# Kernel tuning notes

Hardware: AMD Instinct MI355X
Metric: run time of the kernel (lower is better)

Reference implementation:

```python
import jax, jax.numpy as jnp
import numpy as np

B, N, D = 1, 4096, 3072
H, DH = 16, 64
INNER = H * DH  # 1024
SCALE = DH ** -0.5
EPS = 1e-5


def setup_inputs() -> dict:
    key = jax.random.key(0)
    ks = jax.random.split(key, 4)
    x = jax.random.normal(ks[0], (B, N, D), jnp.float32)
    pe = jax.random.normal(ks[1], (1, 1, N, DH // 2, 2, 2), jnp.float32)
    w_qkv = jax.random.normal(ks[2], (3 * INNER, D), jnp.float32) * 0.02
    w_out = jax.random.normal(ks[3], (D, INNER), jnp.float32) * 0.02
    ln_g = jnp.ones((D,), jnp.float32)
    ln_b = jnp.zeros((D,), jnp.float32)
    return {"x": x, "pe": pe, "w_qkv": w_qkv, "w_out": w_out, "ln_g": ln_g, "ln_b": ln_b}


def _apply_rope(t, pe):
    # t: [b,h,n,d], pe: [1,1,n,d/2,2,2] (Flux rope layout)
    b, h, n, d = t.shape
    t_ = t.reshape(b, h, n, d // 2, 1, 2)
    out = pe[..., 0] * t_[..., 0] + pe[..., 1] * t_[..., 1]  # [b,h,n,d/2,2]
    return out.reshape(b, h, n, d)


def reference(x, pe, w_qkv, w_out, ln_g, ln_b):
    # LayerNorm (norm2)
    mu = jnp.mean(x, axis=-1, keepdims=True)
    var = jnp.mean((x - mu) ** 2, axis=-1, keepdims=True)
    xn = (x - mu) / jnp.sqrt(var + EPS) * ln_g + ln_b
    # QKV projection (no bias)
    qkv = xn @ w_qkv.T  # [b,n,3*inner]
    q, k, v = jnp.split(qkv, 3, axis=-1)
    def split_heads(t):
        return t.reshape(B, N, H, DH).transpose(0, 2, 1, 3)  # b h n d
    q, k, v = split_heads(q), split_heads(k), split_heads(v)
    # RoPE on q and k (attention_aug_bbox with mask=None, aug idx = -1 -> plain rope attn)
    q = _apply_rope(q, pe)
    k = _apply_rope(k, pe)
    scores = jnp.einsum('bhqd,bhkd->bhqk', q, k) * SCALE
    attn = jax.nn.softmax(scores, axis=-1)
    o = jnp.einsum('bhqk,bhkd->bhqd', attn, v)
    o = o.transpose(0, 2, 1, 3).reshape(B, N, INNER)  # b n (h d)
    return o @ w_out.T  # [b,n,dim]
```

## Files before the change

### kernel.cpp

```cpp
#include <hip/hip_runtime.h>
#include <hip/hip_bf16.h>

typedef unsigned short u16;
typedef __attribute__((ext_vector_type(8))) short bf16x8;
typedef __attribute__((ext_vector_type(4))) float f32x4;

#define N_TOK 4096
#define DMODEL 3072
#define NH 16
#define DHEAD 64
#define INNER 1024
#define SCALE_LOG2E 0.18033688011112042f

__device__ __forceinline__ u16 f2bf(float f) {
    union { float f; unsigned u; } un; un.f = f;
    unsigned r = un.u + 0x7fffu + ((un.u >> 16) & 1u);
    return (u16)(r >> 16);
}
__device__ __forceinline__ float bf2f(u16 u) {
    union { unsigned u; float f; } x; x.u = ((unsigned)u) << 16; return x.f;
}
__device__ __forceinline__ unsigned pk2bf(float a, float b) {
    union { float f; unsigned u; } ua, ub; ua.f = a; ub.f = b;
    return __builtin_amdgcn_perm(ub.u + 0x8000u, ua.u + 0x8000u, 0x07060302u);
}
__device__ __forceinline__ void load_lds16(const u16* g, u16* l) {
    __builtin_amdgcn_global_load_lds(
        (const __attribute__((address_space(1))) unsigned int*)g,
        (__attribute__((address_space(3))) unsigned int*)l, 16, 0, 0);
}

__global__ __launch_bounds__(256) void ln_kernel(const float* __restrict__ x,
                                                 const float* __restrict__ g,
                                                 const float* __restrict__ b,
                                                 u16* __restrict__ xn) {
    int row = blockIdx.x;
    int tid = threadIdx.x;
    const float4* xr = (const float4*)(x + (size_t)row * DMODEL);
    float4 v[3];
    float s = 0.f, ss = 0.f;
#pragma unroll
    for (int i = 0; i < 3; ++i) {
        v[i] = xr[i * 256 + tid];
        s  += v[i].x + v[i].y + v[i].z + v[i].w;
        ss += v[i].x * v[i].x + v[i].y * v[i].y + v[i].z * v[i].z + v[i].w * v[i].w;
    }
#pragma unroll
    for (int off = 32; off; off >>= 1) {
        s  += __shfl_xor(s, off);
        ss += __shfl_xor(ss, off);
    }
    __shared__ float red[8];
    int wid = tid >> 6, lane = tid & 63;
    if (lane == 0) { red[wid] = s; red[wid + 4] = ss; }
    __syncthreads();
    s  = red[0] + red[1] + red[2] + red[3];
    ss = red[4] + red[5] + red[6] + red[7];
    float mean = s * (1.f / DMODEL);
    float var  = ss * (1.f / DMODEL) - mean * mean;
    float rstd = rsqrtf(var + 1e-5f);
    ushort4* orow = (ushort4*)(xn + (size_t)row * DMODEL);
#pragma unroll
    for (int i = 0; i < 3; ++i) {
        float4 gg = ((const float4*)g)[i * 256 + tid];
        float4 bb = ((const float4*)b)[i * 256 + tid];
        ushort4 o;
        o.x = f2bf((v[i].x - mean) * rstd * gg.x + bb.x);
        o.y = f2bf((v[i].y - mean) * rstd * gg.y + bb.y);
        o.z = f2bf((v[i].z - mean) * rstd * gg.z + bb.z);
        o.w = f2bf((v[i].w - mean) * rstd * gg.w + bb.w);
        orow[i * 256 + tid] = o;
    }
}

__global__ __launch_bounds__(256) void cvt_bf16(const float* __restrict__ in,
                                                u16* __restrict__ out, int n4) {
    int i = blockIdx.x * 256 + threadIdx.x;
    if (i < n4) {
        float4 v = ((const float4*)in)[i];
        ushort4 o;
        o.x = f2bf(v.x); o.y = f2bf(v.y); o.z = f2bf(v.z); o.w = f2bf(v.w);
        ((ushort4*)out)[i] = o;
    }
}


#define VM6 asm volatile("s_waitcnt vmcnt(6)" ::: "memory")
#define VM0 asm volatile("s_waitcnt vmcnt(0)" ::: "memory")
#define LGK8 asm volatile("s_waitcnt lgkmcnt(8)" ::: "memory")
#define NOPS ((void)0)

#define ST_A(d, h, t) do { \
    load_lds16(pA##h##0 + (size_t)(t) * 64, &lds[(d) * 16384 + (h) * 8192 + dq]); \
    load_lds16(pA##h##1 + (size_t)(t) * 64, &lds[(d) * 16384 + (h) * 8192 + dq + 512]); \
  } while (0)
#define ST_B(d, h, t) do { \
    load_lds16(pB##h##0 + (size_t)(t) * 64, &lds[32768 + (d) * 16384 + (h) * 8192 + dq]); \
    load_lds16(pB##h##1 + (size_t)(t) * 64, &lds[32768 + (d) * 16384 + (h) * 8192 + dq + 512]); \
  } while (0)

#define PHASE(d, p, STAGE, PRE, POST) do { \
    bf16x8 afr[2][2]; \
    if ((p) == 0) { \
      _Pragma("unroll") for (int nf = 0; nf < 4; ++nf) { \
        bfr[nf][0] = *(const bf16x8*)&lds[(d) * 16384 + baseB + nf * 1024 + c0]; \
        bfr[nf][1] = *(const bf16x8*)&lds[(d) * 16384 + baseB + nf * 1024 + c1]; \
      } \
    } \
    _Pragma("unroll") for (int mfl = 0; mfl < 2; ++mfl) { \
      afr[mfl][0] = *(const bf16x8*)&lds[(d) * 16384 + (p) * 4096 + mfl * 1024 + baseA + c0]; \
      afr[mfl][1] = *(const bf16x8*)&lds[(d) * 16384 + (p) * 4096 + mfl * 1024 + baseA + c1]; \
    } \
    STAGE; \
    PRE; \
    __builtin_amdgcn_s_barrier(); \
    asm volatile("s_waitcnt lgkmcnt(0)" ::: "memory"); \
    __builtin_amdgcn_sched_barrier(0); \
    __builtin_amdgcn_s_setprio(1); \
    _Pragma("unroll") for (int mfl = 0; mfl < 2; ++mfl) \
      _Pragma("unroll") for (int nf = 0; nf < 4; ++nf) { \
        acc[(p) * 2 + mfl][nf] = __builtin_amdgcn_mfma_f32_16x16x32_bf16(afr[mfl][0], bfr[nf][0], acc[(p) * 2 + mfl][nf], 0, 0, 0); \
        acc[(p) * 2 + mfl][nf] = __builtin_amdgcn_mfma_f32_16x16x32_bf16(afr[mfl][1], bfr[nf][1], acc[(p) * 2 + mfl][nf], 0, 0, 0); \
      } \
    __builtin_amdgcn_s_setprio(0); \
    POST; \
    __builtin_amdgcn_s_barrier(); \
  } while (0)

template <int CBF16>
__global__ __launch_bounds__(512, 2) void gemm256(const u16* __restrict__ A,
                                                  const u16* __restrict__ B,
                                                  void* __restrict__ C,
                                                  int M, int Nn, int K) {
    __shared__ u16 lds[65536];
    const int tid = threadIdx.x;
    const int lane = tid & 63, wid = tid >> 6;
    const int wm = wid >> 2, wn = wid & 3;
    const int l15 = lane & 15, quad = lane >> 4;
    const int sw = l15 & 7;

    int nbx = Nn >> 8;
    int cpx = gridDim.x >> 3;
    int wg = (blockIdx.x & 7) * cpx + (blockIdx.x >> 3);
    int m0 = (wg / nbx) << 8, n0 = (wg % nbx) << 8;

    const int baseA = wm * 2048 + l15 * 64;
    const int baseB = 32768 + wn * 4096 + l15 * 64;
    const int c0 = (quad ^ sw) * 8;
    const int c1 = ((4 + quad) ^ sw) * 8;
    const int dq = wid * 1024;

    const u16 *pA00, *pA01, *pA10, *pA11, *pB00, *pB01, *pB10, *pB11;
    {
        int scol = ((lane & 7) ^ (lane >> 3)) * 8;
#define MKSRC(h, j, PA, PB) { \
        int ell = (h) * 128 + (wid * 2 + (j)) * 8 + (lane >> 3); \
        int g = ell >> 6, wmh = (ell >> 5) & 1, r = ell & 31; \
        PA = A + (size_t)(m0 + wmh * 128 + g * 32 + r) * K + scol; \
        PB = B + (size_t)(n0 + ell) * K + scol; }
        MKSRC(0, 0, pA00, pB00) MKSRC(0, 1, pA01, pB01)
        MKSRC(1, 0, pA10, pB10) MKSRC(1, 1, pA11, pB11)
#undef MKSRC
    }

    f32x4 acc[8][4];
    f32x4 zero4 = {0.f, 0.f, 0.f, 0.f};
#pragma unroll
    for (int i = 0; i < 8; ++i)
#pragma unroll
        for (int j = 0; j < 4; ++j) acc[i][j] = zero4;
    bf16x8 bfr[4][2];

    ST_B(0, 0, 0); ST_B(0, 1, 0); ST_A(0, 0, 0); ST_A(0, 1, 0);
    ST_B(1, 0, 1); ST_B(1, 1, 1); ST_A(1, 0, 1);
    VM6;
    __builtin_amdgcn_s_barrier();

    const int NIT = (K >> 7) - 1;
    for (int i = 0; i < NIT; ++i) {
        int t = 2 * i;
        PHASE(0, 0, ST_A(1, 1, t + 1), LGK8, NOPS);
        PHASE(0, 1, ST_B(0, 0, t + 2), NOPS, NOPS);
        PHASE(0, 2, ST_B(0, 1, t + 2), NOPS, NOPS);
        PHASE(0, 3, ST_A(0, 0, t + 2), NOPS, VM6);
        PHASE(1, 0, ST_A(0, 1, t + 2), LGK8, NOPS);
        PHASE(1, 1, ST_B(1, 0, t + 3), NOPS, NOPS);
        PHASE(1, 2, ST_B(1, 1, t + 3), NOPS, NOPS);
        PHASE(1, 3, ST_A(1, 0, t + 3), NOPS, VM6);
    }
    {
        int T = K >> 6;
        PHASE(0, 0, ST_A(1, 1, T - 1), LGK8, NOPS);
        PHASE(0, 1, NOPS, NOPS, NOPS);
        PHASE(0, 2, NOPS, NOPS, NOPS);
        PHASE(0, 3, NOPS, NOPS, VM0);
        PHASE(1, 0, NOPS, LGK8, NOPS);
        PHASE(1, 1, NOPS, NOPS, NOPS);
        PHASE(1, 2, NOPS, NOPS, NOPS);
        PHASE(1, 3, NOPS, NOPS, NOPS);
    }

#pragma unroll
    for (int mf = 0; mf < 8; ++mf)
#pragma unroll
        for (int nf = 0; nf < 4; ++nf)
#pragma unroll
            for (int r = 0; r < 4; ++r) {
                int rr = m0 + wm * 128 + mf * 16 + quad * 4 + r;
                int cc = n0 + wn * 64 + nf * 16 + l15;
                if (CBF16)
                    ((u16*)C)[(size_t)rr * Nn + cc] = f2bf(acc[mf][nf][r]);
                else
                    ((float*)C)[(size_t)rr * Nn + cc] = acc[mf][nf][r];
            }
}

__global__ __launch_bounds__(256) void rope_qk(const u16* __restrict__ qkv,
                                               const float* __restrict__ pe,
                                               u16* __restrict__ Qr,
                                               u16* __restrict__ Kr) {
    int n = blockIdx.x;
    int tid = threadIdx.x;
    const u16* qrow = qkv + (size_t)n * DMODEL;
    const float4* pen = (const float4*)(pe + (size_t)n * 128);
#pragma unroll
    for (int it = 0; it < 2; ++it) {
        int p = it * 256 + tid;
        int h = p >> 5, i = p & 31;
        float4 w = pen[i];
        size_t obase = ((size_t)h * N_TOK + n) * DHEAD + 2 * i;
        unsigned qq = *(const unsigned*)&qrow[h * 64 + 2 * i];
        float q0 = bf2f((u16)qq), q1 = bf2f((u16)(qq >> 16));
        *(unsigned*)&Qr[obase] = pk2bf((w.x * q0 + w.y * q1) * SCALE_LOG2E,
                                       (w.z * q0 + w.w * q1) * SCALE_LOG2E);
        unsigned kk = *(const unsigned*)&qrow[INNER + h * 64 + 2 * i];
        float k0 = bf2f((u16)kk), k1 = bf2f((u16)(kk >> 16));
        *(unsigned*)&Kr[obase] = pk2bf(w.x * k0 + w.y * k1, w.z * k0 + w.w * k1);
    }
}

__global__ __launch_bounds__(256) void v_transpose(const u16* __restrict__ qkv,
                                                   u16* __restrict__ Vt) {
    __shared__ u16 t[64][65];
    int n0 = blockIdx.x * 64;
    int h = blockIdx.y;
    int tid = threadIdx.x;
#pragma unroll
    for (int it = 0; it < 4; ++it) {
        int nr = it * 16 + (tid >> 4);
        int dc = (tid & 15) * 4;
        ushort4 v = *(const ushort4*)&qkv[(size_t)(n0 + nr) * DMODEL + 2 * INNER + h * 64 + dc];
        t[dc + 0][nr] = v.x; t[dc + 1][nr] = v.y; t[dc + 2][nr] = v.z; t[dc + 3][nr] = v.w;
    }
    __syncthreads();
#pragma unroll
    for (int it = 0; it < 4; ++it) {
        int dr = it * 16 + (tid >> 4);
        int nc = (tid & 15) * 4;
        ushort4 v;
        v.x = t[dr][nc]; v.y = t[dr][nc + 1]; v.z = t[dr][nc + 2]; v.w = t[dr][nc + 3];
        *(ushort4*)&Vt[((size_t)h * 64 + dr) * N_TOK + n0 + nc] = v;
    }
}

__global__ __launch_bounds__(256, 2) void flash_attn(const u16* __restrict__ Q,
                                                     const u16* __restrict__ K,
                                                     const u16* __restrict__ Vt,
                                                     u16* __restrict__ O) {
    __shared__ u16 lds_all[16384];
    u16* Ks = lds_all;
    u16* Vs = lds_all + 4096;
    int tid = threadIdx.x, lane = tid & 63, wid = tid >> 6;
    u16* Ps = lds_all + 8192 + wid * 2048;
    int l15 = lane & 15, quad = lane >> 4;
    int sw = l15 & 7;
    int h = blockIdx.y;
    int q0 = blockIdx.x * 128 + wid * 32;
    const u16* Qh = Q + (size_t)h * N_TOK * DHEAD;
    const u16* Kh = K + (size_t)h * N_TOK * DHEAD;
    const u16* Vh = Vt + (size_t)h * DHEAD * N_TOK;

    f32x4 zero4 = {0.f, 0.f, 0.f, 0.f};
    bf16x8 ones;
#pragma unroll
    for (int i = 0; i < 8; ++i) ones[i] = (short)0x3F80;

    bf16x8 aq[2][2];
#pragma unroll
    for (int mtQ = 0; mtQ < 2; ++mtQ)
#pragma unroll
        for (int kc = 0; kc < 2; ++kc)
            aq[mtQ][kc] = *(const bf16x8*)&Qh[(size_t)(q0 + mtQ * 16 + l15) * DHEAD + kc * 32 + quad * 8];

    f32x4 o[2][4], lacc[2];
#pragma unroll
    for (int mtQ = 0; mtQ < 2; ++mtQ) {
#pragma unroll
        for (int dt = 0; dt < 4; ++dt) o[mtQ][dt] = zero4;
        lacc[mtQ] = zero4;
    }

    int rbase = wid * 16;
    int rowoff = lane >> 3;
    int csw = ((lane & 7) ^ rowoff) * 8;

    for (int kt = 0; kt < N_TOK; kt += 64) {
        load_lds16(&Kh[(size_t)(kt + rbase + rowoff) * DHEAD + csw], &Ks[rbase * 64]);
        load_lds16(&Kh[(size_t)(kt + rbase + 8 + rowoff) * DHEAD + csw], &Ks[(rbase + 8) * 64]);
        load_lds16(&Vh[(size_t)(rbase + rowoff) * N_TOK + kt + csw], &Vs[rbase * 64]);
        load_lds16(&Vh[(size_t)(rbase + 8 + rowoff) * N_TOK + kt + csw], &Vs[(rbase + 8) * 64]);
        __syncthreads();

        bf16x8 bk[4][2], av[4][2];
#pragma unroll
        for (int t = 0; t < 4; ++t)
#pragma unroll
            for (int kc = 0; kc < 2; ++kc) {
                int off = (t * 16 + l15) * 64 + (((kc * 4 + quad) ^ sw) * 8);
                bk[t][kc] = *(const bf16x8*)&Ks[off];
                av[t][kc] = *(const bf16x8*)&Vs[off];
            }
        __syncthreads();

#pragma unroll
        for (int mtQ = 0; mtQ < 2; ++mtQ) {
            f32x4 s[4];
#pragma unroll
            for (int ntK = 0; ntK < 4; ++ntK) {
                f32x4 t0 = __builtin_amdgcn_mfma_f32_16x16x32_bf16(bk[ntK][0], aq[mtQ][0], zero4, 0, 0, 0);
                s[ntK] = __builtin_amdgcn_mfma_f32_16x16x32_bf16(bk[ntK][1], aq[mtQ][1], t0, 0, 0, 0);
            }
#pragma unroll
            for (int ntK = 0; ntK < 4; ++ntK) {
                uint2 pv;
                pv.x = pk2bf(__builtin_amdgcn_exp2f(s[ntK][0]), __builtin_amdgcn_exp2f(s[ntK][1]));
                pv.y = pk2bf(__builtin_amdgcn_exp2f(s[ntK][2]), __builtin_amdgcn_exp2f(s[ntK][3]));
                int pc = (ntK * 2 + (quad >> 1)) ^ sw;
                *(uint2*)&Ps[(mtQ * 16 + l15) * 64 + pc * 8 + (quad & 1) * 4] = pv;
            }
            bf16x8 bp0 = *(const bf16x8*)&Ps[(mtQ * 16 + l15) * 64 + ((quad ^ sw) * 8)];
            bf16x8 bp1 = *(const bf16x8*)&Ps[(mtQ * 16 + l15) * 64 + (((4 + quad) ^ sw) * 8)];
            lacc[mtQ] = __builtin_amdgcn_mfma_f32_16x16x32_bf16(ones, bp0, lacc[mtQ], 0, 0, 0);
            lacc[mtQ] = __builtin_amdgcn_mfma_f32_16x16x32_bf16(ones, bp1, lacc[mtQ], 0, 0, 0);
#pragma unroll
            for (int dt = 0; dt < 4; ++dt) {
                o[mtQ][dt] = __builtin_amdgcn_mfma_f32_16x16x32_bf16(av[dt][0], bp0, o[mtQ][dt], 0, 0, 0);
                o[mtQ][dt] = __builtin_amdgcn_mfma_f32_16x16x32_bf16(av[dt][1], bp1, o[mtQ][dt], 0, 0, 0);
            }
        }
    }

    __syncthreads();
    u16* scratch = lds_all + wid * 2048;
#pragma unroll
    for (int mtQ = 0; mtQ < 2; ++mtQ) {
        float rl = 1.f / lacc[mtQ][0];
#pragma unroll
        for (int dt = 0; dt < 4; ++dt) {
            uint2 ov;
            ov.x = pk2bf(o[mtQ][dt][0] * rl, o[mtQ][dt][1] * rl);
            ov.y = pk2bf(o[mtQ][dt][2] * rl, o[mtQ][dt][3] * rl);
            *(uint2*)&scratch[(mtQ * 16 + l15) * 64 + dt * 16 + quad * 4] = ov;
        }
    }
#pragma unroll
    for (int p = 0; p < 4; ++p) {
        int q_local = p * 8 + (lane >> 3);
        int dcol = (lane & 7) * 8;
        bf16x8 v = *(const bf16x8*)&scratch[q_local * 64 + dcol];
        *(bf16x8*)&O[(size_t)(q0 + q_local) * INNER + h * 64 + dcol] = v;
    }
}

extern "C" void kernel_launch(void* const* d_in, const int* in_sizes, int n_in,
                              void* d_out, int out_size, void* d_ws, size_t ws_size,
                              hipStream_t stream) {
    const float* x     = (const float*)d_in[0];
    const float* pe    = (const float*)d_in[1];
    const float* w_qkv = (const float*)d_in[2];
    const float* w_out = (const float*)d_in[3];
    const float* ln_g  = (const float*)d_in[4];
    const float* ln_b  = (const float*)d_in[5];
    float* out = (float*)d_out;

    char* ws = (char*)d_ws;
    u16* xn  = (u16*)ws;  ws += (size_t)N_TOK * DMODEL * 2;
    u16* wq  = (u16*)ws;  ws += (size_t)3 * INNER * DMODEL * 2;
    u16* wo  = (u16*)ws;  ws += (size_t)DMODEL * INNER * 2;
    u16* qkv = (u16*)ws;  ws += (size_t)N_TOK * DMODEL * 2;
    u16* Qr  = (u16*)ws;  ws += (size_t)NH * N_TOK * DHEAD * 2;
    u16* Kr  = (u16*)ws;  ws += (size_t)NH * N_TOK * DHEAD * 2;
    u16* Vt  = (u16*)ws;  ws += (size_t)NH * DHEAD * N_TOK * 2;
    u16* Ob  = (u16*)ws;  ws += (size_t)N_TOK * INNER * 2;

    ln_kernel<<<N_TOK, 256, 0, stream>>>(x, ln_g, ln_b, xn);
    {
        int n4 = 3 * INNER * DMODEL / 4;
        cvt_bf16<<<(n4 + 255) / 256, 256, 0, stream>>>(w_qkv, wq, n4);
    }
    {
        int n4 = DMODEL * INNER / 4;
        cvt_bf16<<<(n4 + 255) / 256, 256, 0, stream>>>(w_out, wo, n4);
    }
    gemm256<1><<<dim3((N_TOK / 256) * (DMODEL / 256)), 512, 0, stream>>>(xn, wq, qkv, N_TOK, DMODEL, DMODEL);
    rope_qk<<<N_TOK, 256, 0, stream>>>(qkv, pe, Qr, Kr);
    v_transpose<<<dim3(N_TOK / 64, NH), 256, 0, stream>>>(qkv, Vt);
    flash_attn<<<dim3(N_TOK / 128, NH), 256, 0, stream>>>(Qr, Kr, Vt, Ob);
    gemm256<0><<<dim3((N_TOK / 256) * (DMODEL / 256)), 512, 0, stream>>>(Ob, wo, out, N_TOK, DMODEL, INNER);
}
```

Before: 375.4 us.

## Double-buffer K/V tiles in flash attention with async prefetch

Flash attention now uses two LDS buffers for K/V tiles and prefetches the tile two steps ahead while the current tile is computed. Explicit vmcnt and lgkmcnt waits with raw s_barrier calls replace the two __syncthreads per iteration. The goal is to hide global-to-LDS load latency behind the MFMA and exp work. LDS usage grows from 32KB to 48KB per block, which could limit occupancy at two blocks per CU.

```diff
diff --git a/kernel.cpp b/kernel.cpp
--- a/kernel.cpp
+++ b/kernel.cpp
@@ -86,6 +86,7 @@
 
 
 #define VM6 asm volatile("s_waitcnt vmcnt(6)" ::: "memory")
+#define VM4 asm volatile("s_waitcnt vmcnt(4)" ::: "memory")
 #define VM0 asm volatile("s_waitcnt vmcnt(0)" ::: "memory")
 #define LGK8 asm volatile("s_waitcnt lgkmcnt(8)" ::: "memory")
 #define NOPS ((void)0)
@@ -263,15 +264,61 @@
     }
 }
 
+
+#define FA_STAGE(d, kt) do { \
+    load_lds16(&Kh[(size_t)((kt) + rbase + rowoff) * DHEAD + csw], &lds_all[(d) * 8192 + rbase * 64]); \
+    load_lds16(&Kh[(size_t)((kt) + rbase + 8 + rowoff) * DHEAD + csw], &lds_all[(d) * 8192 + (rbase + 8) * 64]); \
+    load_lds16(&Vh[(size_t)(rbase + rowoff) * N_TOK + (kt) + csw], &lds_all[(d) * 8192 + 4096 + rbase * 64]); \
+    load_lds16(&Vh[(size_t)(rbase + 8 + rowoff) * N_TOK + (kt) + csw], &lds_all[(d) * 8192 + 4096 + (rbase + 8) * 64]); \
+  } while (0)
+
+#define FA_TILE(d, STAGE_STMT, WAIT_STMT) do { \
+    bf16x8 bk[4][2], av[4][2]; \
+    _Pragma("unroll") for (int tt = 0; tt < 4; ++tt) \
+      _Pragma("unroll") for (int kc = 0; kc < 2; ++kc) { \
+        int off = (d) * 8192 + (tt * 16 + l15) * 64 + (((kc * 4 + quad) ^ sw) * 8); \
+        bk[tt][kc] = *(const bf16x8*)&lds_all[off]; \
+        av[tt][kc] = *(const bf16x8*)&lds_all[off + 4096]; \
+      } \
+    asm volatile("s_waitcnt lgkmcnt(0)" ::: "memory"); \
+    __builtin_amdgcn_sched_barrier(0); \
+    __builtin_amdgcn_s_barrier(); \
+    __builtin_amdgcn_sched_barrier(0); \
+    STAGE_STMT; \
+    _Pragma("unroll") for (int mtQ = 0; mtQ < 2; ++mtQ) { \
+      f32x4 s[4]; \
+      _Pragma("unroll") for (int ntK = 0; ntK < 4; ++ntK) { \
+        f32x4 t0 = __builtin_amdgcn_mfma_f32_16x16x32_bf16(bk[ntK][0], aq[mtQ][0], zero4, 0, 0, 0); \
+        s[ntK] = __builtin_amdgcn_mfma_f32_16x16x32_bf16(bk[ntK][1], aq[mtQ][1], t0, 0, 0, 0); \
+      } \
+      _Pragma("unroll") for (int ntK = 0; ntK < 4; ++ntK) { \
+        uint2 pv; \
+        pv.x = pk2bf(__builtin_amdgcn_exp2f(s[ntK][0]), __builtin_amdgcn_exp2f(s[ntK][1])); \
+        pv.y = pk2bf(__builtin_amdgcn_exp2f(s[ntK][2]), __builtin_amdgcn_exp2f(s[ntK][3])); \
+        int pc = (ntK * 2 + (quad >> 1)) ^ sw; \
+        *(uint2*)&Ps[(mtQ * 16 + l15) * 64 + pc * 8 + (quad & 1) * 4] = pv; \
+      } \
+      bf16x8 bp0 = *(const bf16x8*)&Ps[(mtQ * 16 + l15) * 64 + ((quad ^ sw) * 8)]; \
+      bf16x8 bp1 = *(const bf16x8*)&Ps[(mtQ * 16 + l15) * 64 + (((4 + quad) ^ sw) * 8)]; \
+      lacc[mtQ] = __builtin_amdgcn_mfma_f32_16x16x32_bf16(ones, bp0, lacc[mtQ], 0, 0, 0); \
+      lacc[mtQ] = __builtin_amdgcn_mfma_f32_16x16x32_bf16(ones, bp1, lacc[mtQ], 0, 0, 0); \
+      _Pragma("unroll") for (int dt = 0; dt < 4; ++dt) { \
+        o[mtQ][dt] = __builtin_amdgcn_mfma_f32_16x16x32_bf16(av[dt][0], bp0, o[mtQ][dt], 0, 0, 0); \
+        o[mtQ][dt] = __builtin_amdgcn_mfma_f32_16x16x32_bf16(av[dt][1], bp1, o[mtQ][dt], 0, 0, 0); \
+      } \
+    } \
+    WAIT_STMT; \
+    __builtin_amdgcn_s_barrier(); \
+    __builtin_amdgcn_sched_barrier(0); \
+  } while (0)
+
 __global__ __launch_bounds__(256, 2) void flash_attn(const u16* __restrict__ Q,
                                                      const u16* __restrict__ K,
                                                      const u16* __restrict__ Vt,
                                                      u16* __restrict__ O) {
-    __shared__ u16 lds_all[16384];
-    u16* Ks = lds_all;
-    u16* Vs = lds_all + 4096;
+    __shared__ u16 lds_all[24576];
     int tid = threadIdx.x, lane = tid & 63, wid = tid >> 6;
-    u16* Ps = lds_all + 8192 + wid * 2048;
+    u16* Ps = lds_all + 16384 + wid * 2048;
     int l15 = lane & 15, quad = lane >> 4;
     int sw = l15 & 7;
     int h = blockIdx.y;
@@ -304,51 +351,18 @@
     int rowoff = lane >> 3;
     int csw = ((lane & 7) ^ rowoff) * 8;
 
-    for (int kt = 0; kt < N_TOK; kt += 64) {
-        load_lds16(&Kh[(size_t)(kt + rbase + rowoff) * DHEAD + csw], &Ks[rbase * 64]);
-        load_lds16(&Kh[(size_t)(kt + rbase + 8 + rowoff) * DHEAD + csw], &Ks[(rbase + 8) * 64]);
-        load_lds16(&Vh[(size_t)(rbase + rowoff) * N_TOK + kt + csw], &Vs[rbase * 64]);
-        load_lds16(&Vh[(size_t)(rbase + 8 + rowoff) * N_TOK + kt + csw], &Vs[(rbase + 8) * 64]);
-        __syncthreads();
-
-        bf16x8 bk[4][2], av[4][2];
-#pragma unroll
-        for (int t = 0; t < 4; ++t)
-#pragma unroll
-            for (int kc = 0; kc < 2; ++kc) {
-                int off = (t * 16 + l15) * 64 + (((kc * 4 + quad) ^ sw) * 8);
-                bk[t][kc] = *(const bf16x8*)&Ks[off];
-                av[t][kc] = *(const bf16x8*)&Vs[off];
-            }
-        __syncthreads();
-
-#pragma unroll
-        for (int mtQ = 0; mtQ < 2; ++mtQ) {
-            f32x4 s[4];
-#pragma unroll
-            for (int ntK = 0; ntK < 4; ++ntK) {
-                f32x4 t0 = __builtin_amdgcn_mfma_f32_16x16x32_bf16(bk[ntK][0], aq[mtQ][0], zero4, 0, 0, 0);
-                s[ntK] = __builtin_amdgcn_mfma_f32_16x16x32_bf16(bk[ntK][1], aq[mtQ][1], t0, 0, 0, 0);
-            }
-#pragma unroll
-            for (int ntK = 0; ntK < 4; ++ntK) {
-                uint2 pv;
-                pv.x = pk2bf(__builtin_amdgcn_exp2f(s[ntK][0]), __builtin_amdgcn_exp2f(s[ntK][1]));
-                pv.y = pk2bf(__builtin_amdgcn_exp2f(s[ntK][2]), __builtin_amdgcn_exp2f(s[ntK][3]));
-                int pc = (ntK * 2 + (quad >> 1)) ^ sw;
-                *(uint2*)&Ps[(mtQ * 16 + l15) * 64 + pc * 8 + (quad & 1) * 4] = pv;
-            }
-            bf16x8 bp0 = *(const bf16x8*)&Ps[(mtQ * 16 + l15) * 64 + ((quad ^ sw) * 8)];
-            bf16x8 bp1 = *(const bf16x8*)&Ps[(mtQ * 16 + l15) * 64 + (((4 + quad) ^ sw) * 8)];
-            lacc[mtQ] = __builtin_amdgcn_mfma_f32_16x16x32_bf16(ones, bp0, lacc[mtQ], 0, 0, 0);
-            lacc[mtQ] = __builtin_amdgcn_mfma_f32_16x16x32_bf16(ones, bp1, lacc[mtQ], 0, 0, 0);
-#pragma unroll
-            for (int dt = 0; dt < 4; ++dt) {
-                o[mtQ][dt] = __builtin_amdgcn_mfma_f32_16x16x32_bf16(av[dt][0], bp0, o[mtQ][dt], 0, 0, 0);
-                o[mtQ][dt] = __builtin_amdgcn_mfma_f32_16x16x32_bf16(av[dt][1], bp1, o[mtQ][dt], 0, 0, 0);
-            }
-        }
-    }
+    FA_STAGE(0, 0);
+    FA_STAGE(1, 64);
+    VM4;
+    __builtin_amdgcn_s_barrier();
+    __builtin_amdgcn_sched_barrier(0);
+
+    for (int t = 0; t < 62; t += 2) {
+        FA_TILE(0, FA_STAGE(0, (t + 2) * 64), VM4);
+        FA_TILE(1, FA_STAGE(1, (t + 3) * 64), VM4);
+    }
+    FA_TILE(0, NOPS, VM0);
+    FA_TILE(1, NOPS, NOPS);
 
     __syncthreads();
     u16* scratch = lds_all + wid * 2048;
```

Result: faster. 361.6 us (-3.7%).
